# Performance work log

Measured on AMD Instinct MI355X. Metric: run time of the kernel, lower is better.

Reference implementation:

```python
import jax, jax.numpy as jnp
import numpy as np
from jax import lax

STRIDE = (1, 1)
PADDING = ((1, 1), (1, 1))
DILATION = (1, 1)
GROUPS = 1


def setup_inputs() -> dict:
    key = jax.random.key(0)
    k1, k2, k3, k4, k5 = jax.random.split(key, 5)
    # quantized int8-ish activations/weights stored as float (as in the torch module)
    x = jax.random.randint(k1, (32, 128, 56, 56), -128, 128).astype(jnp.float32)
    weight_int = jax.random.randint(k2, (256, 128, 3, 3), -128, 128).astype(jnp.float32)
    bias_int = jax.random.randint(k3, (256,), -1024, 1024).astype(jnp.float32)
    A = jax.random.randint(k4, (256,), 1, 32768)  # per-channel requant multiplier
    N = jax.random.randint(k5, (256,), 16, 25)    # per-channel shift
    return {
        "x": x,
        "weight_int": weight_int,
        "bias_int": bias_int,
        "A": A,
        "N": N,
        "out_min": 0,
        "out_max": 255,
    }


def reference(x, weight_int, bias_int, A, N, out_min, out_max):
    # emulate torch's x.int().float() truncation casts
    xq = jnp.trunc(x)
    wq = jnp.trunc(weight_int)
    bq = jnp.trunc(bias_int)
    out = lax.conv_general_dilated(
        xq, wq,
        window_strides=STRIDE,
        padding=PADDING,
        rhs_dilation=DILATION,
        feature_group_count=GROUPS,
        dimension_numbers=("NCHW", "OIHW", "NCHW"),
    )
    out = jnp.round(out + bq[None, :, None, None])
    # out *= A ; out >>= N  (torch float rshift == divide by 2**N)
    Af = A.astype(jnp.float32)[None, :, None, None]
    Nf = N.astype(jnp.float32)[None, :, None, None]
    out = out * Af / jnp.exp2(Nf)
    if out_min >= 0:
        out = jnp.clip(jnp.round(out), float(out_min), float(out_max))
    return out
```

## Files before the change

### kernel.cpp

```cpp
#include <hip/hip_runtime.h>
#include <stdint.h>

typedef int   v4i  __attribute__((ext_vector_type(4)));
typedef int   v16i __attribute__((ext_vector_type(16)));
typedef float v4f  __attribute__((ext_vector_type(4)));

#define XT_H_STRIDE (66*128)
#define XT_N_STRIDE (58*66*128)
#define XT_BYTES    (32*58*66*128)
#define WQ_BYTES    (256*1152)

__device__ __forceinline__ void gload16(const void* g, void* l) {
  __builtin_amdgcn_global_load_lds(
      (const __attribute__((address_space(1))) void*)g,
      (__attribute__((address_space(3))) void*)l, 16, 0, 0);
}

__global__ __launch_bounds__(256) void xform_x(const float* __restrict__ x,
                                               char* __restrict__ xt) {
  __shared__ int LB[56 * 33];
  int bid = blockIdx.x;
  int n  = bid / 58;
  int hp = bid - n * 58;
  int t  = threadIdx.x;
  int srch = hp - 1;
  bool rowok = (srch >= 0) && (srch < 56);
  char* dstrow = xt + (size_t)n * XT_N_STRIDE + (size_t)hp * XT_H_STRIDE;

  if (rowok) {
    const float* rb = x + ((size_t)(n * 128) * 56 + srch) * 56;
#pragma unroll
    for (int u0 = 0; u0 < 2; ++u0) {
      int u  = t + u0 * 256;
      int wb = u & 15;
      int cb = u >> 4;
      int w0 = wb * 4, ci0 = cb * 4;
      if (w0 < 56) {
        int dw[4] = {0, 0, 0, 0};
#pragma unroll
        for (int i = 0; i < 4; ++i) {
          v4f f = *(const v4f*)(rb + (size_t)(ci0 + i) * 3136 + w0);
#pragma unroll
          for (int j = 0; j < 4; ++j)
            dw[j] |= (((int)f[j]) & 255) << (8 * i);
        }
#pragma unroll
        for (int j = 0; j < 4; ++j)
          LB[(w0 + j) * 33 + cb] = dw[j];
      }
    }
    __syncthreads();
    for (int c = t; c < 528; c += 256) {
      int wp  = c >> 3;
      int cio = c & 7;
      int srw = wp - 1;
      v4i v = {0, 0, 0, 0};
      if (srw >= 0 && srw < 56) {
#pragma unroll
        for (int k = 0; k < 4; ++k) v[k] = LB[srw * 33 + cio * 4 + k];
      }
      *(v4i*)(dstrow + c * 16) = v;
    }
  } else {
    v4i z = {0, 0, 0, 0};
    for (int c = t; c < 528; c += 256) *(v4i*)(dstrow + c * 16) = z;
  }
}

__global__ __launch_bounds__(256) void xform_w(const float* __restrict__ wsrc,
                                               const int* __restrict__ Aq,
                                               const int* __restrict__ Nq,
                                               char* __restrict__ wq2,
                                               float* __restrict__ scale) {
  int idx = blockIdx.x * 256 + threadIdx.x;
  int co = idx / 1152;
  int k  = idx - co * 1152;
  int g  = k >> 7;
  int ci = k & 127;
  int kh = g / 3;
  int kw = g - 3 * kh;
  float f = wsrc[(size_t)(co * 128 + ci) * 9 + kh * 3 + kw];
  int kt    = g * 4 + (ci >> 5);
  int chunk = (ci >> 4) & 1;
  wq2[((kt * 2 + chunk) * 256 + co) * 16 + (ci & 15)] = (signed char)(int)f;
  if (idx < 256) {
    scale[idx] = (float)Aq[idx] * exp2f(-(float)Nq[idx]);
  }
}

__global__ __launch_bounds__(256, 2) void qconv_gemm(
    const char* __restrict__ xt, const char* __restrict__ wq2,
    const float* __restrict__ bias, const float* __restrict__ scale,
    const int* __restrict__ pmin, const int* __restrict__ pmax,
    float* __restrict__ out) {
  __shared__ __align__(16) char Bp[4 * 8448];
  __shared__ __align__(16) char As[2][8192];

  int bid = blockIdx.x;
  int xcd = bid & 7;
  int nt  = xcd * 112 + (bid >> 3);
  int n   = nt / 28;
  int ht  = nt - n * 28;
  int h0  = ht * 2;

  int t   = threadIdx.x;
  int wv  = t >> 6;
  int ln  = t & 63;
  int l31 = ln & 31;
  int hi  = ln >> 5;
  int wm  = wv & 1, wn = wv >> 1;

  const char* wbase = wq2;
  const char* xb    = xt + (size_t)n * XT_N_STRIDE + (size_t)h0 * XT_H_STRIDE;

  for (int it = 0; it < 9; ++it) {
    int s = t + it * 256;
    if (s < 2112) {
      int row = s / 528;
      int rr  = s - row * 528;
      int w   = rr >> 3;
      int cq  = rr & 7;
      gload16(xb + row * XT_H_STRIDE + w * 128 + ((cq ^ (w & 7)) << 4),
              Bp + it * 4096 + wv * 1024);
    }
  }
  gload16(wbase + t * 16, &As[0][wv * 1024]);
  gload16(wbase + 4096 + t * 16, &As[0][4096 + wv * 1024]);
  asm volatile("s_waitcnt vmcnt(0)" ::: "memory");
  asm volatile("s_barrier" ::: "memory");

  v16i acc[4][2];
#pragma unroll
  for (int i = 0; i < 4; ++i)
#pragma unroll
    for (int j = 0; j < 2; ++j) {
      v16i z = {0};
      acc[i][j] = z;
    }

  for (int kt = 0; kt < 36; ++kt) {
    int p   = kt & 1;
    int g   = kt >> 2;
    int c32 = kt & 3;
    int kh  = g / 3;
    int kw  = g - 3 * kh;

    asm volatile("s_barrier" ::: "memory");
    if (kt < 35) {
      const char* wkt = wbase + (kt + 1) * 8192;
      gload16(wkt + t * 16, &As[1 - p][wv * 1024]);
      gload16(wkt + 4096 + t * 16, &As[1 - p][4096 + wv * 1024]);
      asm volatile("s_waitcnt vmcnt(2)" ::: "memory");
    } else {
      asm volatile("s_waitcnt vmcnt(0)" ::: "memory");
    }
    asm volatile("s_barrier" ::: "memory");

    const char* abase = As[p] + hi * 4096 + (wm * 128 + l31) * 16;
    int bswz = ((((c32 << 1) + hi) ^ ((l31 + kw) & 7)) << 4);
    const char* bbase = Bp + (wn + kh) * XT_H_STRIDE + (l31 + kw) * 128 + bswz;

    v4i a[4], b[2];
#pragma unroll
    for (int fi = 0; fi < 4; ++fi)
      a[fi] = *(const v4i*)(abase + fi * 512);
#pragma unroll
    for (int fj = 0; fj < 2; ++fj)
      b[fj] = *(const v4i*)(bbase + fj * 4096);
#pragma unroll
    for (int fi = 0; fi < 4; ++fi)
#pragma unroll
      for (int fj = 0; fj < 2; ++fj)
        acc[fi][fj] = __builtin_amdgcn_mfma_i32_32x32x32_i8(a[fi], b[fj], acc[fi][fj], 0, 0, 0);
  }

  float mn = (float)pmin[0];
  float mx = (float)pmax[0];
#pragma unroll
  for (int fi = 0; fi < 4; ++fi) {
#pragma unroll
    for (int rg = 0; rg < 16; ++rg) {
      int co = wm * 128 + fi * 32 + (rg & 3) + 8 * (rg >> 2) + 4 * hi;
      float bs = bias[co];
      float sc = scale[co];
      size_t obase = ((size_t)(n * 256 + co) * 56 + (h0 + wn)) * 56;
#pragma unroll
      for (int fj = 0; fj < 2; ++fj) {
        int w = fj * 32 + l31;
        if (w < 56) {
          float f = (float)acc[fi][fj][rg] + bs;
          f = rintf(f * sc);
          f = fminf(fmaxf(f, mn), mx);
          out[obase + w] = f;
        }
      }
    }
  }
}

extern "C" void kernel_launch(void* const* d_in, const int* in_sizes, int n_in,
                              void* d_out, int out_size, void* d_ws, size_t ws_size,
                              hipStream_t stream) {
  const float* x  = (const float*)d_in[0];
  const float* w  = (const float*)d_in[1];
  const float* b  = (const float*)d_in[2];
  const int*   Aq = (const int*)d_in[3];
  const int*   Nq = (const int*)d_in[4];
  const int*   mn = (const int*)d_in[5];
  const int*   mx = (const int*)d_in[6];
  float* out = (float*)d_out;

  char*  xt    = (char*)d_ws;
  char*  wq2   = xt + XT_BYTES;
  float* scale = (float*)(wq2 + WQ_BYTES);

  hipLaunchKernelGGL(xform_x, dim3(32 * 58), dim3(256), 0, stream, x, xt);
  hipLaunchKernelGGL(xform_w, dim3(1152), dim3(256), 0, stream, w, Aq, Nq, wq2, scale);
  hipLaunchKernelGGL(qconv_gemm, dim3(896), dim3(256), 0, stream,
                     xt, wq2, b, scale, mn, mx, out);
}
```

Measured before the change: 212.4 us.

## Split output channels across blocks and read weights directly from global into registers

Halves the output-channel tile per block (128 instead of 256) and doubles the grid. Weight tiles are no longer staged through LDS with barriers; each lane loads its A fragments directly from a re-laid-out weight buffer in global memory. The K loop is unrolled two MFMAs per step with register double-buffering of A and B, and s_setprio is raised around the MFMAs. This removes the per-iteration barriers and LDS traffic for weights, at the cost of duplicating the input-row LDS load across two blocks and adding global-load latency inside the loop.

```diff
diff --git a/kernel.cpp b/kernel.cpp
--- a/kernel.cpp
+++ b/kernel.cpp
@@ -80,28 +80,28 @@
   int kh = g / 3;
   int kw = g - 3 * kh;
   float f = wsrc[(size_t)(co * 128 + ci) * 9 + kh * 3 + kw];
-  int kt    = g * 4 + (ci >> 5);
-  int chunk = (ci >> 4) & 1;
-  wq2[((kt * 2 + chunk) * 256 + co) * 16 + (ci & 15)] = (signed char)(int)f;
+  wq2[((k >> 6) * 256 + co) * 64 + (k & 63)] = (signed char)(int)f;
   if (idx < 256) {
     scale[idx] = (float)Aq[idx] * exp2f(-(float)Nq[idx]);
   }
 }
 
-__global__ __launch_bounds__(256, 2) void qconv_gemm(
+__global__ __launch_bounds__(256, 3) void qconv_gemm(
     const char* __restrict__ xt, const char* __restrict__ wq2,
     const float* __restrict__ bias, const float* __restrict__ scale,
     const int* __restrict__ pmin, const int* __restrict__ pmax,
     float* __restrict__ out) {
   __shared__ __align__(16) char Bp[4 * 8448];
-  __shared__ __align__(16) char As[2][8192];
 
   int bid = blockIdx.x;
   int xcd = bid & 7;
-  int nt  = xcd * 112 + (bid >> 3);
+  int q   = bid >> 3;
+  int mt  = q & 1;
+  int nt  = xcd * 112 + (q >> 1);
   int n   = nt / 28;
   int ht  = nt - n * 28;
   int h0  = ht * 2;
+  int m0  = mt * 128;
 
   int t   = threadIdx.x;
   int wv  = t >> 6;
@@ -110,8 +110,8 @@
   int hi  = ln >> 5;
   int wm  = wv & 1, wn = wv >> 1;
 
-  const char* wbase = wq2;
-  const char* xb    = xt + (size_t)n * XT_N_STRIDE + (size_t)h0 * XT_H_STRIDE;
+  const char* xb = xt + (size_t)n * XT_N_STRIDE + (size_t)h0 * XT_H_STRIDE;
+  const char* abase = wq2 + (size_t)(m0 + wm * 64 + l31) * 64 + hi * 16;
 
   for (int it = 0; it < 9; ++it) {
     int s = t + it * 256;
@@ -124,63 +124,84 @@
               Bp + it * 4096 + wv * 1024);
     }
   }
-  gload16(wbase + t * 16, &As[0][wv * 1024]);
-  gload16(wbase + 4096 + t * 16, &As[0][4096 + wv * 1024]);
-  asm volatile("s_waitcnt vmcnt(0)" ::: "memory");
-  asm volatile("s_barrier" ::: "memory");
-
-  v16i acc[4][2];
-#pragma unroll
-  for (int i = 0; i < 4; ++i)
+
+  v4i a[4], b[4], an[4], bn[4];
+#pragma unroll
+  for (int fi = 0; fi < 2; ++fi)
+#pragma unroll
+    for (int kk = 0; kk < 2; ++kk)
+      a[fi * 2 + kk] = *(const v4i*)(abase + fi * 2048 + kk * 32);
+
+  __syncthreads();
+
+  {
+    const char* bb = Bp + wn * XT_H_STRIDE + l31 * 128;
+    int sm = l31 & 7;
+#pragma unroll
+    for (int fj = 0; fj < 2; ++fj)
+#pragma unroll
+      for (int kk = 0; kk < 2; ++kk)
+        b[fj * 2 + kk] = *(const v4i*)(bb + fj * 4096 + (((kk << 1) + hi) ^ sm) * 16);
+  }
+
+  v16i acc[2][2];
+#pragma unroll
+  for (int i = 0; i < 2; ++i)
 #pragma unroll
     for (int j = 0; j < 2; ++j) {
       v16i z = {0};
       acc[i][j] = z;
     }
 
-  for (int kt = 0; kt < 36; ++kt) {
-    int p   = kt & 1;
-    int g   = kt >> 2;
-    int c32 = kt & 3;
-    int kh  = g / 3;
-    int kw  = g - 3 * kh;
-
-    asm volatile("s_barrier" ::: "memory");
-    if (kt < 35) {
-      const char* wkt = wbase + (kt + 1) * 8192;
-      gload16(wkt + t * 16, &As[1 - p][wv * 1024]);
-      gload16(wkt + 4096 + t * 16, &As[1 - p][4096 + wv * 1024]);
-      asm volatile("s_waitcnt vmcnt(2)" ::: "memory");
-    } else {
-      asm volatile("s_waitcnt vmcnt(0)" ::: "memory");
-    }
-    asm volatile("s_barrier" ::: "memory");
-
-    const char* abase = As[p] + hi * 4096 + (wm * 128 + l31) * 16;
-    int bswz = ((((c32 << 1) + hi) ^ ((l31 + kw) & 7)) << 4);
-    const char* bbase = Bp + (wn + kh) * XT_H_STRIDE + (l31 + kw) * 128 + bswz;
-
-    v4i a[4], b[2];
-#pragma unroll
-    for (int fi = 0; fi < 4; ++fi)
-      a[fi] = *(const v4i*)(abase + fi * 512);
-#pragma unroll
-    for (int fj = 0; fj < 2; ++fj)
-      b[fj] = *(const v4i*)(bbase + fj * 4096);
-#pragma unroll
-    for (int fi = 0; fi < 4; ++fi)
+#pragma unroll
+  for (int kt = 0; kt < 18; ++kt) {
+    if (kt < 17) {
+      int kn  = kt + 1;
+      int pn  = kn & 1;
+      int gn  = kn >> 1;
+      int khn = gn / 3;
+      int kwn = gn - 3 * khn;
+      const char* ak = abase + (size_t)kn * 16384;
+#pragma unroll
+      for (int fi = 0; fi < 2; ++fi)
+#pragma unroll
+        for (int kk = 0; kk < 2; ++kk)
+          an[fi * 2 + kk] = *(const v4i*)(ak + fi * 2048 + kk * 32);
+      const char* bbn = Bp + (wn + khn) * XT_H_STRIDE + (l31 + kwn) * 128;
+      int smn = (l31 + kwn) & 7;
 #pragma unroll
       for (int fj = 0; fj < 2; ++fj)
-        acc[fi][fj] = __builtin_amdgcn_mfma_i32_32x32x32_i8(a[fi], b[fj], acc[fi][fj], 0, 0, 0);
+#pragma unroll
+        for (int kk = 0; kk < 2; ++kk)
+          bn[fj * 2 + kk] =
+              *(const v4i*)(bbn + fj * 4096 + ((((pn << 2) + (kk << 1) + hi) ^ smn) * 16));
+    }
+
+    __builtin_amdgcn_s_setprio(1);
+#pragma unroll
+    for (int fi = 0; fi < 2; ++fi)
+#pragma unroll
+      for (int fj = 0; fj < 2; ++fj) {
+        acc[fi][fj] = __builtin_amdgcn_mfma_i32_32x32x32_i8(a[fi * 2 + 0], b[fj * 2 + 0],
+                                                            acc[fi][fj], 0, 0, 0);
+        acc[fi][fj] = __builtin_amdgcn_mfma_i32_32x32x32_i8(a[fi * 2 + 1], b[fj * 2 + 1],
+                                                            acc[fi][fj], 0, 0, 0);
+      }
+    __builtin_amdgcn_s_setprio(0);
+
+    if (kt < 17) {
+#pragma unroll
+      for (int u = 0; u < 4; ++u) { a[u] = an[u]; b[u] = bn[u]; }
+    }
   }
 
   float mn = (float)pmin[0];
   float mx = (float)pmax[0];
 #pragma unroll
-  for (int fi = 0; fi < 4; ++fi) {
+  for (int fi = 0; fi < 2; ++fi) {
 #pragma unroll
     for (int rg = 0; rg < 16; ++rg) {
-      int co = wm * 128 + fi * 32 + (rg & 3) + 8 * (rg >> 2) + 4 * hi;
+      int co = m0 + wm * 64 + fi * 32 + (rg & 3) + 8 * (rg >> 2) + 4 * hi;
       float bs = bias[co];
       float sc = scale[co];
       size_t obase = ((size_t)(n * 256 + co) * 56 + (h0 + wn)) * 56;
@@ -216,6 +237,6 @@
 
   hipLaunchKernelGGL(xform_x, dim3(32 * 58), dim3(256), 0, stream, x, xt);
   hipLaunchKernelGGL(xform_w, dim3(1152), dim3(256), 0, stream, w, Aq, Nq, wq2, scale);
-  hipLaunchKernelGGL(qconv_gemm, dim3(896), dim3(256), 0, stream,
+  hipLaunchKernelGGL(qconv_gemm, dim3(1792), dim3(256), 0, stream,
                      xt, wq2, b, scale, mn, mx, out);
 }
```

New measurement: 195.2 us. -8.1%, faster.

## Double K-step per iteration with software-pipelined LDS fragment loads

Applied to the files above, without the earlier changes.

Repacks the weight workspace so each pipeline stage covers 64 K elements, split by M-half and chunk. The GEMM loop drops from 36 to 18 iterations with one barrier each instead of two. Within each iteration, A and B fragments for the next sub-step are prefetched from LDS while the MFMAs run, paced by explicit lgkmcnt waits, sched_barrier and setprio. The goal is to cut barrier and LDS latency stalls, at the cost of twice the A-tile LDS and more registers, which may reduce occupancy.

```diff
diff --git a/kernel.cpp b/kernel.cpp
--- a/kernel.cpp
+++ b/kernel.cpp
@@ -70,7 +70,7 @@
 __global__ __launch_bounds__(256) void xform_w(const float* __restrict__ wsrc,
                                                const int* __restrict__ Aq,
                                                const int* __restrict__ Nq,
-                                               char* __restrict__ wq2,
+                                               char* __restrict__ wq3,
                                                float* __restrict__ scale) {
   int idx = blockIdx.x * 256 + threadIdx.x;
   int co = idx / 1152;
@@ -80,21 +80,24 @@
   int kh = g / 3;
   int kw = g - 3 * kh;
   float f = wsrc[(size_t)(co * 128 + ci) * 9 + kh * 3 + kw];
-  int kt    = g * 4 + (ci >> 5);
-  int chunk = (ci >> 4) & 1;
-  wq2[((kt * 2 + chunk) * 256 + co) * 16 + (ci & 15)] = (signed char)(int)f;
+  int kt    = k >> 6;
+  int mhalf = co >> 7;
+  int chunk = (k >> 4) & 3;
+  int row   = co & 127;
+  int col   = k & 15;
+  wq3[(((kt * 2 + mhalf) * 4 + chunk) * 128 + row) * 16 + col] = (signed char)(int)f;
   if (idx < 256) {
     scale[idx] = (float)Aq[idx] * exp2f(-(float)Nq[idx]);
   }
 }
 
 __global__ __launch_bounds__(256, 2) void qconv_gemm(
-    const char* __restrict__ xt, const char* __restrict__ wq2,
+    const char* __restrict__ xt, const char* __restrict__ wq3,
     const float* __restrict__ bias, const float* __restrict__ scale,
     const int* __restrict__ pmin, const int* __restrict__ pmax,
     float* __restrict__ out) {
   __shared__ __align__(16) char Bp[4 * 8448];
-  __shared__ __align__(16) char As[2][8192];
+  __shared__ __align__(16) char As[2][16384];
 
   int bid = blockIdx.x;
   int xcd = bid & 7;
@@ -110,8 +113,7 @@
   int hi  = ln >> 5;
   int wm  = wv & 1, wn = wv >> 1;
 
-  const char* wbase = wq2;
-  const char* xb    = xt + (size_t)n * XT_N_STRIDE + (size_t)h0 * XT_H_STRIDE;
+  const char* xb = xt + (size_t)n * XT_N_STRIDE + (size_t)h0 * XT_H_STRIDE;
 
   for (int it = 0; it < 9; ++it) {
     int s = t + it * 256;
@@ -124,10 +126,24 @@
               Bp + it * 4096 + wv * 1024);
     }
   }
-  gload16(wbase + t * 16, &As[0][wv * 1024]);
-  gload16(wbase + 4096 + t * 16, &As[0][4096 + wv * 1024]);
+#pragma unroll
+  for (int ps = 0; ps < 4; ++ps)
+    gload16(wq3 + ps * 4096 + t * 16, As[0] + ps * 4096 + wv * 1024);
+
   asm volatile("s_waitcnt vmcnt(0)" ::: "memory");
   asm volatile("s_barrier" ::: "memory");
+
+  const int aoff = wm * 8192 + hi * 2048 + l31 * 16;
+
+  v4i af[2], ag[2], b[4], bn[4];
+  {
+    const char* bb = Bp + wn * XT_H_STRIDE + l31 * 128;
+    int sm = l31 & 7;
+    b[0] = *(const v4i*)(bb + (((0 + hi) ^ sm) << 4));
+    b[1] = *(const v4i*)(bb + (((2 + hi) ^ sm) << 4));
+    b[2] = *(const v4i*)(bb + 4096 + (((0 + hi) ^ sm) << 4));
+    b[3] = *(const v4i*)(bb + 4096 + (((2 + hi) ^ sm) << 4));
+  }
 
   v16i acc[4][2];
 #pragma unroll
@@ -138,40 +154,85 @@
       acc[i][j] = z;
     }
 
-  for (int kt = 0; kt < 36; ++kt) {
-    int p   = kt & 1;
-    int g   = kt >> 2;
-    int c32 = kt & 3;
-    int kh  = g / 3;
-    int kw  = g - 3 * kh;
-
-    asm volatile("s_barrier" ::: "memory");
-    if (kt < 35) {
-      const char* wkt = wbase + (kt + 1) * 8192;
-      gload16(wkt + t * 16, &As[1 - p][wv * 1024]);
-      gload16(wkt + 4096 + t * 16, &As[1 - p][4096 + wv * 1024]);
-      asm volatile("s_waitcnt vmcnt(2)" ::: "memory");
+#pragma unroll
+  for (int kt = 0; kt < 18; ++kt) {
+    const int cur = kt & 1;
+    const char* ap = As[cur];
+
+    if (kt < 17) {
+      const char* src = wq3 + (size_t)(kt + 1) * 16384;
+      char* dst = As[cur ^ 1];
+#pragma unroll
+      for (int ps = 0; ps < 4; ++ps)
+        gload16(src + ps * 4096 + t * 16, dst + ps * 4096 + wv * 1024);
+    }
+    af[0] = *(const v4i*)(ap + aoff);
+    af[1] = *(const v4i*)(ap + aoff + 4096);
+    ag[0] = *(const v4i*)(ap + aoff + 1 * 512);
+    ag[1] = *(const v4i*)(ap + aoff + 4096 + 1 * 512);
+    asm volatile("s_waitcnt lgkmcnt(2)" ::: "memory");
+    __builtin_amdgcn_sched_barrier(0);
+    __builtin_amdgcn_s_setprio(1);
+    acc[0][0] = __builtin_amdgcn_mfma_i32_32x32x32_i8(af[0], b[0], acc[0][0], 0, 0, 0);
+    acc[0][0] = __builtin_amdgcn_mfma_i32_32x32x32_i8(af[1], b[1], acc[0][0], 0, 0, 0);
+    acc[0][1] = __builtin_amdgcn_mfma_i32_32x32x32_i8(af[0], b[2], acc[0][1], 0, 0, 0);
+    acc[0][1] = __builtin_amdgcn_mfma_i32_32x32x32_i8(af[1], b[3], acc[0][1], 0, 0, 0);
+    __builtin_amdgcn_s_setprio(0);
+    af[0] = ag[0]; af[1] = ag[1];
+
+    ag[0] = *(const v4i*)(ap + aoff + 2 * 512);
+    ag[1] = *(const v4i*)(ap + aoff + 4096 + 2 * 512);
+    asm volatile("s_waitcnt lgkmcnt(2)" ::: "memory");
+    __builtin_amdgcn_sched_barrier(0);
+    __builtin_amdgcn_s_setprio(1);
+    acc[1][0] = __builtin_amdgcn_mfma_i32_32x32x32_i8(af[0], b[0], acc[1][0], 0, 0, 0);
+    acc[1][0] = __builtin_amdgcn_mfma_i32_32x32x32_i8(af[1], b[1], acc[1][0], 0, 0, 0);
+    acc[1][1] = __builtin_amdgcn_mfma_i32_32x32x32_i8(af[0], b[2], acc[1][1], 0, 0, 0);
+    acc[1][1] = __builtin_amdgcn_mfma_i32_32x32x32_i8(af[1], b[3], acc[1][1], 0, 0, 0);
+    __builtin_amdgcn_s_setprio(0);
+    af[0] = ag[0]; af[1] = ag[1];
+
+    ag[0] = *(const v4i*)(ap + aoff + 3 * 512);
+    ag[1] = *(const v4i*)(ap + aoff + 4096 + 3 * 512);
+    if (kt < 17) {
+      const int kn  = kt + 1;
+      const int pn  = kn & 1;
+      const int gn  = kn >> 1;
+      const int khn = gn / 3;
+      const int kwn = gn - 3 * khn;
+      const char* bbn = Bp + (wn + khn) * XT_H_STRIDE + (l31 + kwn) * 128;
+      int smn = (l31 + kwn) & 7;
+      bn[0] = *(const v4i*)(bbn + ((((pn << 2) + 0 + hi) ^ smn) << 4));
+      bn[1] = *(const v4i*)(bbn + ((((pn << 2) + 2 + hi) ^ smn) << 4));
+      bn[2] = *(const v4i*)(bbn + 4096 + ((((pn << 2) + 0 + hi) ^ smn) << 4));
+      bn[3] = *(const v4i*)(bbn + 4096 + ((((pn << 2) + 2 + hi) ^ smn) << 4));
+      asm volatile("s_waitcnt lgkmcnt(6)" ::: "memory");
     } else {
+      asm volatile("s_waitcnt lgkmcnt(2)" ::: "memory");
+    }
+    __builtin_amdgcn_sched_barrier(0);
+    __builtin_amdgcn_s_setprio(1);
+    acc[2][0] = __builtin_amdgcn_mfma_i32_32x32x32_i8(af[0], b[0], acc[2][0], 0, 0, 0);
+    acc[2][0] = __builtin_amdgcn_mfma_i32_32x32x32_i8(af[1], b[1], acc[2][0], 0, 0, 0);
+    acc[2][1] = __builtin_amdgcn_mfma_i32_32x32x32_i8(af[0], b[2], acc[2][1], 0, 0, 0);
+    acc[2][1] = __builtin_amdgcn_mfma_i32_32x32x32_i8(af[1], b[3], acc[2][1], 0, 0, 0);
+    __builtin_amdgcn_s_setprio(0);
+    af[0] = ag[0]; af[1] = ag[1];
+
+    asm volatile("s_waitcnt lgkmcnt(0)" ::: "memory");
+    __builtin_amdgcn_sched_barrier(0);
+    __builtin_amdgcn_s_setprio(1);
+    acc[3][0] = __builtin_amdgcn_mfma_i32_32x32x32_i8(af[0], b[0], acc[3][0], 0, 0, 0);
+    acc[3][0] = __builtin_amdgcn_mfma_i32_32x32x32_i8(af[1], b[1], acc[3][0], 0, 0, 0);
+    acc[3][1] = __builtin_amdgcn_mfma_i32_32x32x32_i8(af[0], b[2], acc[3][1], 0, 0, 0);
+    acc[3][1] = __builtin_amdgcn_mfma_i32_32x32x32_i8(af[1], b[3], acc[3][1], 0, 0, 0);
+    __builtin_amdgcn_s_setprio(0);
+    if (kt < 17) {
+#pragma unroll
+      for (int u = 0; u < 4; ++u) b[u] = bn[u];
       asm volatile("s_waitcnt vmcnt(0)" ::: "memory");
-    }
-    asm volatile("s_barrier" ::: "memory");
-
-    const char* abase = As[p] + hi * 4096 + (wm * 128 + l31) * 16;
-    int bswz = ((((c32 << 1) + hi) ^ ((l31 + kw) & 7)) << 4);
-    const char* bbase = Bp + (wn + kh) * XT_H_STRIDE + (l31 + kw) * 128 + bswz;
-
-    v4i a[4], b[2];
-#pragma unroll
-    for (int fi = 0; fi < 4; ++fi)
-      a[fi] = *(const v4i*)(abase + fi * 512);
-#pragma unroll
-    for (int fj = 0; fj < 2; ++fj)
-      b[fj] = *(const v4i*)(bbase + fj * 4096);
-#pragma unroll
-    for (int fi = 0; fi < 4; ++fi)
-#pragma unroll
-      for (int fj = 0; fj < 2; ++fj)
-        acc[fi][fj] = __builtin_amdgcn_mfma_i32_32x32x32_i8(a[fi], b[fj], acc[fi][fj], 0, 0, 0);
+      asm volatile("s_barrier" ::: "memory");
+    }
   }
 
   float mn = (float)pmin[0];
@@ -211,11 +272,11 @@
   float* out = (float*)d_out;
 
   char*  xt    = (char*)d_ws;
-  char*  wq2   = xt + XT_BYTES;
-  float* scale = (float*)(wq2 + WQ_BYTES);
+  char*  wq3   = xt + XT_BYTES;
+  float* scale = (float*)(wq3 + WQ_BYTES);
 
   hipLaunchKernelGGL(xform_x, dim3(32 * 58), dim3(256), 0, stream, x, xt);
-  hipLaunchKernelGGL(xform_w, dim3(1152), dim3(256), 0, stream, w, Aq, Nq, wq2, scale);
+  hipLaunchKernelGGL(xform_w, dim3(1152), dim3(256), 0, stream, w, Aq, Nq, wq3, scale);
   hipLaunchKernelGGL(qconv_gemm, dim3(896), dim3(256), 0, stream,
-                     xt, wq2, b, scale, mn, mx, out);
-}
+                     xt, wq3, b, scale, mn, mx, out);
+}
```

New measurement: 198.9 us. 6.4% less time.
